# Kernel optimization log

Hardware: AMD Instinct MI355X
Metric: run time of the kernel (lower is better)

The kernel has to match this reference:

```python
import jax, jax.numpy as jnp
import numpy as np

B, C, H, W = 16, 3, 1024, 1024
OUT_HW = 224  # F.interpolate target size before the ResNet backbone
EPS = 1e-8


def setup_inputs() -> dict:
    key = jax.random.key(0)
    images = jax.random.uniform(key, (B, C, H, W), dtype=jnp.float32)
    return {"images": images}


def reference(images):
    # Batched FFT2 over spatial dims (replaces the per-(b,c) CPU numpy loop)
    fft = jnp.fft.fft2(images, axes=(-2, -1))                 # complex64 (B,C,H,W)
    fft = jnp.fft.fftshift(fft, axes=(-2, -1))
    spec = jnp.log1p(jnp.abs(fft))                             # log-magnitude spectrum

    # Per-sample min/max normalization to [0, 1] (flatten over C,H,W)
    b = spec.shape[0]
    flat = spec.reshape(b, -1)
    mn = flat.min(axis=1).reshape(b, 1, 1, 1)
    mx = flat.max(axis=1).reshape(b, 1, 1, 1)
    spec = (spec - mn) / (mx - mn + EPS)

    # Bilinear resize to 224x224; jax.image.resize 'bilinear' uses half-pixel
    # centers, matching torch F.interpolate(align_corners=False).
    out = jax.image.resize(spec, (b, spec.shape[1], OUT_HW, OUT_HW), method='bilinear')
    return out
```

## Files before the change

### kernel.cpp

```cpp
#include <hip/hip_runtime.h>
#include <math.h>

#define N 1024
#define BATCH 16
#define CH 3
#define BC 48
#define OUTHW 224
#define KSCALE (1024.0f / 224.0f)
#define SCALE  (224.0f / 1024.0f)
#define ABYTES ((size_t)BC * N * N * 8)
#define T1OFF  (768 * 2048)
#define SLOTOFF 1802240
#define WBAR() __builtin_amdgcn_wave_barrier()

#define CMUL(dr, di, ar, ai, br, bi) do {                         \
    float _r = (ar) * (br) - (ai) * (bi);                         \
    float _i = (ar) * (bi) + (ai) * (br);                         \
    (dr) = _r; (di) = _i; } while (0)

#define RADIX4(ar,ai,br,bi,cr,ci,dr,di, o0r,o0i,o1r,o1i,o2r,o2i,o3r,o3i) do { \
    float u0r=(ar)+(cr), u0i=(ai)+(ci);                           \
    float u1r=(ar)-(cr), u1i=(ai)-(ci);                           \
    float u2r=(br)+(dr), u2i=(bi)+(di);                           \
    float u3r=(bi)-(di), u3i=(dr)-(br);                           \
    (o0r)=u0r+u2r; (o0i)=u0i+u2i;                                 \
    (o1r)=u1r+u3r; (o1i)=u1i+u3i;                                 \
    (o2r)=u0r-u2r; (o2i)=u0i-u2i;                                 \
    (o3r)=u1r-u3r; (o3i)=u1i-u3i; } while (0)

__device__ __forceinline__ void dft16(float* xr, float* xi) {
  const float W16R[4][4] = {
    {1.f, 1.f, 1.f, 1.f},
    {1.f,  0.9238795325f,  0.7071067812f,  0.3826834324f},
    {1.f,  0.7071067812f,  0.0f,          -0.7071067812f},
    {1.f,  0.3826834324f, -0.7071067812f, -0.9238795325f}};
  const float W16I[4][4] = {
    {0.f, 0.f, 0.f, 0.f},
    {0.f, -0.3826834324f, -0.7071067812f, -0.9238795325f},
    {0.f, -0.7071067812f, -1.0f,          -0.7071067812f},
    {0.f, -0.9238795325f, -0.7071067812f,  0.3826834324f}};
  float tr[16], ti[16];
#pragma unroll
  for (int j = 0; j < 4; ++j) {
    RADIX4(xr[j],xi[j], xr[j+4],xi[j+4], xr[j+8],xi[j+8], xr[j+12],xi[j+12],
           tr[4*j],ti[4*j], tr[4*j+1],ti[4*j+1], tr[4*j+2],ti[4*j+2], tr[4*j+3],ti[4*j+3]);
  }
#pragma unroll
  for (int j = 0; j < 4; ++j) {
    float ar[4], ai_[4];
#pragma unroll
    for (int k = 0; k < 4; ++k) {
      if (j == 0 || k == 0) { ar[k] = tr[j+4*k]; ai_[k] = ti[j+4*k]; }
      else CMUL(ar[k], ai_[k], tr[j+4*k], ti[j+4*k], W16R[j][k], W16I[j][k]);
    }
    RADIX4(ar[0],ai_[0], ar[1],ai_[1], ar[2],ai_[2], ar[3],ai_[3],
           xr[j],xi[j], xr[j+4],xi[j+4], xr[j+8],xi[j+8], xr[j+12],xi[j+12]);
  }
}

__device__ __forceinline__ void stage2(float* xr, float* xi,
                                       const float2* __restrict__ twg, int j2) {
#pragma unroll
  for (int k = 1; k < 16; ++k) {
    float2 w = twg[4 * j2 * k];
    CMUL(xr[k], xi[k], xr[k], xi[k], w.x, w.y);
  }
  dft16(xr, xi);
}

__device__ __forceinline__ void wave_fft1024_1buf(float* xr, float* xi,
                                                  float* wb,
                                                  const float2* __restrict__ twg,
                                                  int l) {
  const int base2 = l + (l >> 4);
  const int j2 = l & 15;
  const int ob = 272 * (l >> 4) + j2;
  dft16(xr, xi);
#pragma unroll
  for (int k = 0; k < 16; ++k) wb[17*l + k] = xr[k];
  WBAR();
#pragma unroll
  for (int k = 0; k < 16; ++k) xr[k] = wb[base2 + 68*k];
  WBAR();
#pragma unroll
  for (int k = 0; k < 16; ++k) wb[17*l + k] = xi[k];
  WBAR();
#pragma unroll
  for (int k = 0; k < 16; ++k) xi[k] = wb[base2 + 68*k];
  WBAR();
  stage2(xr, xi, twg, j2);
#pragma unroll
  for (int k = 0; k < 16; ++k) wb[ob + 17*k] = xr[k];
  WBAR();
#pragma unroll
  for (int m = 0; m < 4; ++m)
#pragma unroll
    for (int k = 0; k < 4; ++k) xr[m + 4*k] = wb[base2 + 68*m + 272*k];
  WBAR();
#pragma unroll
  for (int k = 0; k < 16; ++k) wb[ob + 17*k] = xi[k];
  WBAR();
#pragma unroll
  for (int m = 0; m < 4; ++m)
#pragma unroll
    for (int k = 0; k < 4; ++k) xi[m + 4*k] = wb[base2 + 68*m + 272*k];
  WBAR();
#pragma unroll
  for (int m = 0; m < 4; ++m) {
    float ar[4], ai_[4];
#pragma unroll
    for (int k = 0; k < 4; ++k) { ar[k] = xr[m + 4*k]; ai_[k] = xi[m + 4*k]; }
    const int j = l + 64*m;
#pragma unroll
    for (int k = 1; k < 4; ++k) {
      float2 w = twg[j * k];
      CMUL(ar[k], ai_[k], ar[k], ai_[k], w.x, w.y);
    }
    RADIX4(ar[0],ai_[0], ar[1],ai_[1], ar[2],ai_[2], ar[3],ai_[3],
           xr[m],xi[m], xr[m+4],xi[m+4], xr[m+8],xi[m+8], xr[m+12],xi[m+12]);
  }
}

__global__ void k_init(float2* __restrict__ tw, int* __restrict__ slots) {
  int g = blockIdx.x * 256 + threadIdx.x;
  if (g < 1024) {
    float ang = -6.283185307179586f * ((float)g / 1024.0f);
    float s, c;
    sincosf(ang, &s, &c);
    tw[g] = make_float2(c, s);
    slots[g] = 0x7F800000;
  } else {
    slots[g] = 0;
  }
}

__global__ __launch_bounds__(512, 6) void k_rowfft(const float* __restrict__ in,
                                                   float2* __restrict__ A,
                                                   const float2* __restrict__ twg) {
  __shared__ float lds[8704];
  const int t  = threadIdx.x;
  const int w  = t >> 6;
  const int l  = t & 63;
  const int bc  = blockIdx.x >> 6;
  const int h0b = (blockIdx.x & 63) << 4;
  const int r0  = h0b + 2 * w;
  float* wb = lds + w * 1088;
  const float* row0 = in + ((size_t)bc << 20) + ((size_t)r0 << 10);
  const float* row1 = row0 + N;
  float xr[16], xi[16];
  const float sgn = (l & 1) ? -1.0f : 1.0f;
#pragma unroll
  for (int k = 0; k < 16; ++k) {
    xr[k] =  sgn * row0[l + 64*k];
    xi[k] = -sgn * row1[l + 64*k];
  }
  wave_fft1024_1buf(xr, xi, wb, twg, l);
  float* stre = lds;
  float* stim = lds + 4160;
  const int rr = t & 15, v0 = t >> 4;
  float2* Abc = A + ((size_t)bc << 20);
#pragma unroll
  for (int h = 0; h < 2; ++h) {
    const int slo = (h == 0) ? 0 : 4;
    const int cnt = (h == 0) ? 4 : 5;
    float par[5], pai[5], pbr[5], pbi[5];
    __syncthreads();
#pragma unroll
    for (int s = 0; s < 16; ++s) wb[l + 64*s] = xr[s];
    WBAR();
#pragma unroll
    for (int u = 0; u < 5; ++u) {
      if (u < cnt) {
        int s = slo + u;
        int i = l + 64*s;
        if (i <= 512) {
          float qr = wb[(N - i) & (N - 1)];
          par[u] = 0.5f * (xr[s] + qr);
          pbi[u] = 0.5f * (qr - xr[s]);
        }
      }
    }
    WBAR();
#pragma unroll
    for (int s = 0; s < 16; ++s) wb[l + 64*s] = xi[s];
    WBAR();
#pragma unroll
    for (int u = 0; u < 5; ++u) {
      if (u < cnt) {
        int s = slo + u;
        int i = l + 64*s;
        if (i <= 512) {
          float qi = wb[(N - i) & (N - 1)];
          pai[u] = 0.5f * (xi[s] - qi);
          pbr[u] = 0.5f * (xi[s] + qi);
        }
      }
    }
    __syncthreads();
#pragma unroll
    for (int u = 0; u < 5; ++u) {
      if (u < cnt) {
        int s = slo + u;
        int i = l + 64*s;
        if (i <= 512) {
          int c = i - 256 * h;
          stre[(2*w)     * 260 + c] = par[u]; stim[(2*w)     * 260 + c] = pai[u];
          stre[(2*w + 1) * 260 + c] = pbr[u]; stim[(2*w + 1) * 260 + c] = pbi[u];
        }
      }
    }
    __syncthreads();
#pragma unroll
    for (int i2 = 0; i2 < 9; ++i2) {
      if (i2 < 8 + h) {
        int v = 256 * h + v0 + 32 * i2;
        if (v <= 512) {
          int c = v - 256 * h;
          Abc[(size_t)v * N + h0b + rr] =
              make_float2(stre[rr*260 + c], stim[rr*260 + c]);
        }
      }
    }
  }
}

__global__ __launch_bounds__(256, 8) void k_colfft(const float2* __restrict__ A,
                                                   float* __restrict__ WSf,
                                                   int* __restrict__ slots,
                                                   const float2* __restrict__ twg) {
  __shared__ float lds[4352];
  const int t  = threadIdx.x;
  const int w  = t >> 6;
  const int l  = t & 63;
  const int gw = blockIdx.x * 4 + w;
  const int bc = gw / 513;
  const int sx = gw - bc * 513;
  const int b  = bc / CH;
  float* wb = lds + w * 1088;
  const float2* src = A + ((size_t)bc << 20) + ((size_t)sx << 10);
  float xr[16], xi[16];
#pragma unroll
  for (int k = 0; k < 16; ++k) { float2 v = src[l + 64*k]; xr[k] = v.x; xi[k] = v.y; }
  wave_fft1024_1buf(xr, xi, wb, twg, l);
  float lmin = 3.4e38f, lmax = 0.0f;
#pragma unroll
  for (int s = 0; s < 16; ++s) {
    float sp = __logf(1.0f + sqrtf(xr[s]*xr[s] + xi[s]*xi[s]));
    wb[l + 64*s] = sp;
    lmin = fminf(lmin, sp); lmax = fmaxf(lmax, sp);
  }
#pragma unroll
  for (int off = 32; off; off >>= 1) {
    lmin = fminf(lmin, __shfl_xor(lmin, off));
    lmax = fmaxf(lmax, __shfl_xor(lmax, off));
  }
  if (l == 0) {
    atomicMin(&slots[b * 64 + (sx & 63)],        __float_as_int(lmin));
    atomicMax(&slots[1024 + b * 64 + (sx & 63)], __float_as_int(lmax));
  }
  WBAR();
  float* T1 = WSf + ((size_t)bc << 21) + T1OFF;
  const bool mir = (sx != 0) && (sx != 512);
#pragma unroll
  for (int obk = 0; obk < 4; ++obk) {
    int oh = l + 64 * obk;
    if (oh < OUTHW) {
      float x = ((float)oh + 0.5f) * KSCALE - 0.5f;
      int jlo = (int)ceilf(x - KSCALE);
      float ssum = 0.0f, acc = 0.0f, accm = 0.0f;
#pragma unroll
      for (int u = 0; u < 10; ++u) {
        int j = jlo + u;
        float wgt = 1.0f - fabsf((float)j - x) * SCALE;
        wgt = fmaxf(wgt, 0.0f);
        bool valid = (j >= 0) && (j <= N - 1);
        if (!valid) wgt = 0.0f;
        int ja = valid ? j : 0;
        ssum += wgt;
        acc  += wgt * wb[ja];
        accm += wgt * wb[(N - ja) & (N - 1)];
      }
      float inv = 1.0f / ssum;
      T1[(size_t)sx * OUTHW + oh] = acc * inv;
      if (mir) T1[(size_t)(N - sx) * OUTHW + oh] = accm * inv;
    }
  }
}

__global__ __launch_bounds__(256) void k_resize2(const float2* __restrict__ A,
                                                 const int* __restrict__ slots,
                                                 float* __restrict__ out) {
  __shared__ float s2[2];
  const int ow = blockIdx.x % OUTHW;
  const int bc = blockIdx.x / OUTHW;
  const int b  = bc / CH;
  const int t  = threadIdx.x;
  if (t < 64) {
    int mn = slots[b * 64 + t];
#pragma unroll
    for (int off = 32; off; off >>= 1) mn = min(mn, __shfl_xor(mn, off));
    if (t == 0) s2[0] = __int_as_float(mn);
  } else if (t < 128) {
    int mx = slots[1024 + b * 64 + (t - 64)];
#pragma unroll
    for (int off = 32; off; off >>= 1) mx = max(mx, __shfl_xor(mx, off));
    if (t == 64) s2[1] = __int_as_float(mx);
  }
  __syncthreads();
  if (t >= OUTHW) return;
  const float mn = s2[0];
  const float mx = s2[1];
  const float inv = 1.0f / (mx - mn + 1e-8f);
  const float* T1 = (const float*)(A + ((size_t)bc << 20)) + T1OFF;
  float x = ((float)ow + 0.5f) * KSCALE - 0.5f;
  int jlo = (int)ceilf(x - KSCALE);
  float ssum = 0.0f, acc = 0.0f;
#pragma unroll
  for (int u = 0; u < 10; ++u) {
    int j = jlo + u;
    float wv = 1.0f - fabsf((float)j - x) * SCALE;
    wv = fmaxf(wv, 0.0f);
    bool valid = (j >= 0) && (j <= N - 1);
    if (!valid) wv = 0.0f;
    int ja = valid ? j : 0;
    ssum += wv;
    acc += wv * T1[(size_t)ja * OUTHW + t];
  }
  float v = acc / ssum;
  out[((size_t)bc * OUTHW + t) * OUTHW + ow] = (v - mn) * inv;
}

extern "C" void kernel_launch(void* const* d_in, const int* in_sizes, int n_in,
                              void* d_out, int out_size, void* d_ws, size_t ws_size,
                              hipStream_t stream) {
  const float* in = (const float*)d_in[0];
  float* out = (float*)d_out;
  float2* A = (float2*)d_ws;
  float* WSf = (float*)d_ws;
  float2* twg = (float2*)((char*)d_ws + ABYTES + 128);
  int* slots = (int*)(WSf + SLOTOFF);

  k_init<<<8, 256, 0, stream>>>(twg, slots);
  k_rowfft<<<BC * 64, 512, 0, stream>>>(in, A, twg);
  k_colfft<<<(BC * 513) / 4, 256, 0, stream>>>(A, WSf, slots, twg);
  k_resize2<<<BC * OUTHW, 256, 0, stream>>>(A, slots, out);
}
```

Baseline: 431.9 us.

## Process row/column FFTs in channel groups to keep spectrum workspace cache-resident

Splits the 48 image channels into 4 groups of 12. The row FFT and column FFT kernels now run per group and reuse one smaller spectrum buffer, so the intermediate stays small enough to be served from the large last-level cache rather than HBM. The column-resize output moves to its own region, indexed by global channel, so the final resize kernel still runs once over all channels. In exchange there are more kernel launches with smaller grids, and each launch boundary costs a drain and tail.

```diff
diff --git a/kernel.cpp b/kernel.cpp
--- a/kernel.cpp
+++ b/kernel.cpp
@@ -5,12 +5,16 @@
 #define BATCH 16
 #define CH 3
 #define BC 48
+#define GROUPS 4
+#define GBC 12
 #define OUTHW 224
 #define KSCALE (1024.0f / 224.0f)
 #define SCALE  (224.0f / 1024.0f)
+#define SLABF  2097152
 #define ABYTES ((size_t)BC * N * N * 8)
-#define T1OFF  (768 * 2048)
 #define SLOTOFF 1802240
+#define T1BASE ((size_t)GBC * SLABF)
+#define T1SZ   (OUTHW * N)
 #define WBAR() __builtin_amdgcn_wave_barrier()
 
 #define CMUL(dr, di, ar, ai, br, bi) do {                         \
@@ -141,11 +145,11 @@
   const int t  = threadIdx.x;
   const int w  = t >> 6;
   const int l  = t & 63;
-  const int bc  = blockIdx.x >> 6;
+  const int bcl = blockIdx.x >> 6;
   const int h0b = (blockIdx.x & 63) << 4;
   const int r0  = h0b + 2 * w;
   float* wb = lds + w * 1088;
-  const float* row0 = in + ((size_t)bc << 20) + ((size_t)r0 << 10);
+  const float* row0 = in + ((size_t)bcl << 20) + ((size_t)r0 << 10);
   const float* row1 = row0 + N;
   float xr[16], xi[16];
   const float sgn = (l & 1) ? -1.0f : 1.0f;
@@ -158,7 +162,7 @@
   float* stre = lds;
   float* stim = lds + 4160;
   const int rr = t & 15, v0 = t >> 4;
-  float2* Abc = A + ((size_t)bc << 20);
+  float2* Abc = A + ((size_t)bcl << 20);
 #pragma unroll
   for (int h = 0; h < 2; ++h) {
     const int slo = (h == 0) ? 0 : 4;
@@ -227,17 +231,18 @@
 __global__ __launch_bounds__(256, 8) void k_colfft(const float2* __restrict__ A,
                                                    float* __restrict__ WSf,
                                                    int* __restrict__ slots,
-                                                   const float2* __restrict__ twg) {
+                                                   const float2* __restrict__ twg,
+                                                   int bc0) {
   __shared__ float lds[4352];
   const int t  = threadIdx.x;
   const int w  = t >> 6;
   const int l  = t & 63;
   const int gw = blockIdx.x * 4 + w;
-  const int bc = gw / 513;
-  const int sx = gw - bc * 513;
-  const int b  = bc / CH;
+  const int bcl = gw / 513;
+  const int sx = gw - bcl * 513;
+  const int b  = (bc0 + bcl) / CH;
   float* wb = lds + w * 1088;
-  const float2* src = A + ((size_t)bc << 20) + ((size_t)sx << 10);
+  const float2* src = A + ((size_t)bcl << 20) + ((size_t)sx << 10);
   float xr[16], xi[16];
 #pragma unroll
   for (int k = 0; k < 16; ++k) { float2 v = src[l + 64*k]; xr[k] = v.x; xi[k] = v.y; }
@@ -259,7 +264,7 @@
     atomicMax(&slots[1024 + b * 64 + (sx & 63)], __float_as_int(lmax));
   }
   WBAR();
-  float* T1 = WSf + ((size_t)bc << 21) + T1OFF;
+  float* T1 = WSf + T1BASE + (size_t)(bc0 + bcl) * T1SZ;
   const bool mir = (sx != 0) && (sx != 512);
 #pragma unroll
   for (int obk = 0; obk < 4; ++obk) {
@@ -287,7 +292,7 @@
   }
 }
 
-__global__ __launch_bounds__(256) void k_resize2(const float2* __restrict__ A,
+__global__ __launch_bounds__(256) void k_resize2(const float* __restrict__ WSf,
                                                  const int* __restrict__ slots,
                                                  float* __restrict__ out) {
   __shared__ float s2[2];
@@ -311,7 +316,7 @@
   const float mn = s2[0];
   const float mx = s2[1];
   const float inv = 1.0f / (mx - mn + 1e-8f);
-  const float* T1 = (const float*)(A + ((size_t)bc << 20)) + T1OFF;
+  const float* T1 = WSf + T1BASE + (size_t)bc * T1SZ;
   float x = ((float)ow + 0.5f) * KSCALE - 0.5f;
   int jlo = (int)ceilf(x - KSCALE);
   float ssum = 0.0f, acc = 0.0f;
@@ -341,7 +346,10 @@
   int* slots = (int*)(WSf + SLOTOFF);
 
   k_init<<<8, 256, 0, stream>>>(twg, slots);
-  k_rowfft<<<BC * 64, 512, 0, stream>>>(in, A, twg);
-  k_colfft<<<(BC * 513) / 4, 256, 0, stream>>>(A, WSf, slots, twg);
-  k_resize2<<<BC * OUTHW, 256, 0, stream>>>(A, slots, out);
-}
+  for (int g = 0; g < GROUPS; ++g) {
+    const int bc0 = g * GBC;
+    k_rowfft<<<GBC * 64, 512, 0, stream>>>(in + ((size_t)bc0 << 20), A, twg);
+    k_colfft<<<(GBC * 513) / 4, 256, 0, stream>>>(A, WSf, slots, twg, bc0);
+  }
+  k_resize2<<<BC * OUTHW, 256, 0, stream>>>(WSf, slots, out);
+}
```

After: 487.6 us. 1.13x slower.
